# Optimization experiments

Measured on AMD Instinct MI355X. Metric: run time of the kernel, lower is better.

## Reference

```python
import jax, jax.numpy as jnp
import numpy as np

N, C, H, W = 8, 64, 128, 128
KS = 3


def setup_inputs() -> dict:
    key = jax.random.key(0)
    k1, k2, k3, k4 = jax.random.split(key, 4)
    gr = jax.random.normal(k1, (N, C, H, W), dtype=jnp.float32)
    gt = jax.random.normal(k2, (N, C, H, W), dtype=jnp.float32)
    # Conv2d(in_channel, 9*in_channel, 3, stride=1, pad=1): weight [O, I, kh, kw], bias [O]
    fan_in = C * KS * KS
    bound = 1.0 / np.sqrt(fan_in)
    Wc = jax.random.uniform(k3, (KS * KS * C, C, KS, KS), dtype=jnp.float32, minval=-bound, maxval=bound)
    bc = jax.random.uniform(k4, (KS * KS * C,), dtype=jnp.float32, minval=-bound, maxval=bound)
    return {"gr": gr, "gt": gt, "Wc": Wc, "bc": bc}


def reference(gr, gt, Wc, bc):
    # dynamic_filter = Conv2d(C, 9C, 3, 1, 1)(gt)
    filt = jax.lax.conv_general_dilated(
        gt, Wc, window_strides=(1, 1), padding=((1, 1), (1, 1)),
        dimension_numbers=("NCHW", "OIHW", "NCHW"),
    ) + bc[None, :, None, None]  # [N, 9C, H, W]

    n, c, h, w = gr.shape
    pad = (KS - 1) // 2
    # replicate padding (torch F.pad mode='replicate' == jnp 'edge')
    grp = jnp.pad(gr, ((0, 0), (0, 0), (pad, pad), (pad, pad)), mode="edge")
    # 3x3 patches as 9 shifted views: [N, C, 9, H, W], index order (kh, kw)
    patches = jnp.stack(
        [grp[:, :, i:i + h, j:j + w] for i in range(KS) for j in range(KS)], axis=2
    )
    # torch code's conv output channel layout is (c, kh, kw); its double transpose
    # of both patches and kernels cancels, so pairing is kernel[c, kh, kw] * patch[c, kh, kw]
    k = filt.reshape(n, c, KS * KS, h, w)
    return jnp.sum(patches * k, axis=2)  # [N, C, H, W]
```

## Files before the change

### kernel.cpp

```cpp
#include <hip/hip_runtime.h>
#include <stdint.h>


typedef short bf16x8 __attribute__((ext_vector_type(8)));
typedef float f32x4 __attribute__((ext_vector_type(4)));

#define ROWBLK_B 16640
#define BTAP_B   18432
#define ZERO_OFF 663552
#define GTB_OFF  (ZERO_OFF + ROWBLK_B)

__device__ __forceinline__ uint32_t f2bf(float f) {
  uint32_t x = __float_as_uint(f);
  return (x + 0x7FFFu + ((x >> 16) & 1u)) >> 16;
}
__device__ __forceinline__ float bf2f(uint32_t u) { return __uint_as_float(u << 16); }

__device__ __forceinline__ void gload_lds16(const void* g, void* l) {
  __builtin_amdgcn_global_load_lds(
      (const __attribute__((address_space(1))) void*)g,
      (__attribute__((address_space(3))) void*)l, 16, 0, 0);
}

__global__ void prep_wc(const float* __restrict__ Wc, uint8_t* __restrict__ ws) {
  int ch = blockIdx.x * 256 + threadIdx.x;
  int tb = ch / 1152;
  int cw = ch - tb * 1152;
  int tap = tb >> 2, octile = tb & 3;
  int row = cw >> 3, sl = cw & 7;
  int slot = sl ^ (row & 7);
  int ic0 = slot * 8;
  int oc = octile * 144 + row;
  uint32_t p[4];
#pragma unroll
  for (int e = 0; e < 4; ++e) {
    uint32_t lo = f2bf(Wc[(oc * 64 + ic0 + 2 * e) * 9 + tap]);
    uint32_t hi = f2bf(Wc[(oc * 64 + ic0 + 2 * e + 1) * 9 + tap]);
    p[e] = lo | (hi << 16);
  }
  uint4 u; u.x = p[0]; u.y = p[1]; u.z = p[2]; u.w = p[3];
  *(uint4*)(ws + (size_t)tb * BTAP_B + (size_t)cw * 16) = u;
}

__global__ void prep_gt(const float* __restrict__ gt, uint8_t* __restrict__ ws) {
  int b = blockIdx.x;
  if (b == 1024) {
    uint4 z; z.x = z.y = z.z = z.w = 0;
    for (int i = threadIdx.x; i < 1040; i += 256)
      *(uint4*)(ws + ZERO_OFF + (size_t)i * 16) = z;
    return;
  }
  int n = b >> 7, y = b & 127;
  uint8_t* base = ws + GTB_OFF + (size_t)b * ROWBLK_B;
  for (int i = threadIdx.x; i < 1040; i += 256) {
    int r = i >> 3, sl = i & 7;
    int slot = sl ^ (r & 7);
    uint4 u; u.x = u.y = u.z = u.w = 0;
    if (r >= 1 && r <= 128) {
      int w = r - 1, ic0 = slot * 8;
      uint32_t p[4];
#pragma unroll
      for (int e = 0; e < 4; ++e) {
        uint32_t lo = f2bf(gt[((n * 64 + ic0 + 2 * e) * 128 + y) * 128 + w]);
        uint32_t hi = f2bf(gt[((n * 64 + ic0 + 2 * e + 1) * 128 + y) * 128 + w]);
        p[e] = lo | (hi << 16);
      }
      u.x = p[0]; u.y = p[1]; u.z = p[2]; u.w = p[3];
    }
    *(uint4*)(base + (size_t)i * 16) = u;
  }
}

__global__ __launch_bounds__(512, 2) void dfn_mfma(
    const float* __restrict__ gr, const float* __restrict__ bc,
    const uint8_t* __restrict__ ws, float* __restrict__ out) {
  __shared__ uint8_t smem[156928];
  uint8_t* Abuf = smem;
  uint8_t* Bbuf = smem + 83200;
  const int tid = threadIdx.x;
  const int lane = tid & 63;
  const int wv = tid >> 6;
  const int l15 = lane & 15;
  const int l4 = lane >> 4;
  const int bid = blockIdx.x;
  const int octile = (bid >> 3) & 3;
  const int nh = (bid & 7) | ((bid >> 5) << 3);
  const int n = nh >> 5;
  const int h0 = (nh & 31) * 4;

  f32x4 acc[4][9];
#pragma unroll
  for (int nf = 0; nf < 9; ++nf) {
    float bias = bc[octile * 144 + nf * 16 + l15];
#pragma unroll
    for (int mf = 0; mf < 4; ++mf) {
      acc[mf][nf][0] = bias; acc[mf][nf][1] = bias;
      acc[mf][nf][2] = bias; acc[mf][nf][3] = bias;
    }
  }

  int bo[2], aoff[3][2];
#pragma unroll
  for (int kk = 0; kk < 2; ++kk) {
    bo[kk] = l15 * 128 + ((kk * 64 + l4 * 16) ^ ((l15 & 7) << 4));
#pragma unroll
    for (int dwp = 0; dwp < 3; ++dwp) {
      int rl = l15 + dwp;
      aoff[dwp][kk] = rl * 128 + ((kk * 64 + l4 * 16) ^ ((rl & 7) << 4));
    }
  }
  int mrow[4], mcol[4];
#pragma unroll
  for (int mf = 0; mf < 4; ++mf) {
    mrow[mf] = (wv * 4 + mf) >> 3;
    mcol[mf] = ((wv * 4 + mf) & 7) * 2048;
  }

  const uint8_t* gtb = ws + GTB_OFF;
  const uint8_t* zblk = ws + ZERO_OFF;

#define ISSUE_B(T, BUFI) do {                                                 \
    const uint8_t* bsrc_ = ws + (size_t)((T) * 4 + octile) * BTAP_B;          \
    uint8_t* bdst_ = Bbuf + (BUFI) * BTAP_B;                                  \
    _Pragma("unroll")                                                         \
    for (int it = 0; it < 3; ++it) {                                          \
      int idx = it * 512 + tid;                                               \
      if (idx < 1152)                                                         \
        gload_lds16(bsrc_ + (size_t)idx * 16,                                 \
                    bdst_ + (size_t)(it * 512 + (tid & ~63)) * 16);           \
    }                                                                         \
  } while (0)

#define ISSUE_AROW(Y, SLOT) do {                                              \
    int y_ = (Y);                                                             \
    const uint8_t* src_ = (y_ >= 0 && y_ < 128)                               \
        ? (gtb + (size_t)(n * 128 + y_) * ROWBLK_B) : zblk;                   \
    uint8_t* dst_ = Abuf + (SLOT) * ROWBLK_B;                                 \
    _Pragma("unroll")                                                         \
    for (int it = 0; it < 3; ++it) {                                          \
      int idx = it * 512 + tid;                                               \
      if (idx < 1040)                                                         \
        gload_lds16(src_ + (size_t)idx * 16,                                  \
                    dst_ + (size_t)(it * 512 + (tid & ~63)) * 16);            \
    }                                                                         \
  } while (0)

#define TAP(DH, DWP, BUFI) do {                                               \
    const uint8_t* Bcur_ = Bbuf + (BUFI) * BTAP_B;                            \
    _Pragma("unroll")                                                         \
    for (int kk = 0; kk < 2; ++kk) {                                          \
      bf16x8 afr[4];                                                          \
      _Pragma("unroll")                                                       \
      for (int mf = 0; mf < 4; ++mf) {                                        \
        int idx_ = mrow[mf] + ((DH) + 1);                           \
        int slot_ = (idx_ == 5) ? 0 : idx_;     \
        afr[mf] = *(const bf16x8*)(Abuf + slot_ * ROWBLK_B + mcol[mf]         \
                                   + aoff[DWP][kk]);                          \
      }                                                                       \
      const uint8_t* baddr_ = Bcur_ + bo[kk];                                 \
      bf16x8 bq[4];                                                           \
      _Pragma("unroll")                                                       \
      for (int p = 0; p < 4; ++p)                                             \
        bq[p] = *(const bf16x8*)(baddr_ + p * 2048);                          \
      __builtin_amdgcn_s_setprio(1);                                          \
      _Pragma("unroll")                                                       \
      for (int nf = 0; nf < 9; ++nf) {                                        \
        bf16x8 bcur_ = bq[nf & 3];                                            \
        if (nf + 4 < 9)                                                       \
          bq[nf & 3] = *(const bf16x8*)(baddr_ + (nf + 4) * 2048);            \
        _Pragma("unroll")                                                     \
        for (int mf = 0; mf < 4; ++mf)                                        \
          acc[mf][nf] = __builtin_amdgcn_mfma_f32_16x16x32_bf16(              \
              afr[mf], bcur_, acc[mf][nf], 0, 0, 0);                          \
      }                                                                       \
      __builtin_amdgcn_s_setprio(0);                                          \
    }                                                                         \
  } while (0)

#pragma unroll
  for (int row = 0; row < 5; ++row) ISSUE_AROW(h0 - 1 + row, row);
  ISSUE_B(0, 0);
  ISSUE_B(1, 1);
  __syncthreads();

  ISSUE_B(2, 2); ISSUE_B(3, 3);
  TAP(-1, 0, 0); TAP(-1, 1, 1);
  __syncthreads();
  ISSUE_B(4, 0); ISSUE_B(5, 1);
  TAP(-1, 2, 2); TAP(0, 0, 3);
  __syncthreads();
  ISSUE_B(6, 2); ISSUE_B(7, 3);
  ISSUE_AROW(h0 + 4, 0);
  TAP(0, 1, 0); TAP(0, 2, 1);
  __syncthreads();
  ISSUE_B(8, 0);
  TAP(1, 0, 2); TAP(1, 1, 3);
  __syncthreads();
  TAP(1, 2, 0);
  __syncthreads();

  uint8_t* wreg = smem + wv * 8448;
#pragma unroll
  for (int mf = 0; mf < 4; ++mf) {
#pragma unroll
    for (int nf = 0; nf < 9; ++nf) {
      int ocl = nf * 16 + l15;
      int c = (ocl * 7282) >> 16;
      int k = ocl - c * 9;
      uint8_t* wp = wreg + c * 32 + k * 2;
#pragma unroll
      for (int q = 0; q < 4; ++q) {
        int pix = l4 * 4 + q;
        *(uint16_t*)(wp + pix * 528) = (uint16_t)f2bf(acc[mf][nf][q]);
      }
    }
    asm volatile("s_waitcnt lgkmcnt(0)" ::: "memory");
    __builtin_amdgcn_sched_barrier(0);
    int m = (wv * 4 + mf) * 16 + l15;
    int row = m >> 7, w = m & 127;
    int h = h0 + row;
#pragma unroll
    for (int cc = 0; cc < 4; ++cc) {
      int cl = l4 * 4 + cc;
      const uint8_t* rp = wreg + (size_t)l15 * 528 + cl * 32;
      uint4 v0 = *(const uint4*)rp;
      uint32_t v1 = *(const uint32_t*)(rp + 16);
      float fk[9];
      fk[0] = bf2f(v0.x & 0xffff); fk[1] = bf2f(v0.x >> 16);
      fk[2] = bf2f(v0.y & 0xffff); fk[3] = bf2f(v0.y >> 16);
      fk[4] = bf2f(v0.z & 0xffff); fk[5] = bf2f(v0.z >> 16);
      fk[6] = bf2f(v0.w & 0xffff); fk[7] = bf2f(v0.w >> 16);
      fk[8] = bf2f(v1 & 0xffff);
      int cg = octile * 16 + cl;
      const float* grc = gr + (size_t)(n * 64 + cg) * 16384;
      float s = 0.f;
#pragma unroll
      for (int i = 0; i < 3; ++i) {
        int yy = h + i - 1; yy = yy < 0 ? 0 : (yy > 127 ? 127 : yy);
#pragma unroll
        for (int j = 0; j < 3; ++j) {
          int xx = w + j - 1; xx = xx < 0 ? 0 : (xx > 127 ? 127 : xx);
          s = fmaf(fk[i * 3 + j], grc[yy * 128 + xx], s);
        }
      }
      out[(size_t)(n * 64 + cg) * 16384 + h * 128 + w] = s;
    }
    asm volatile("s_waitcnt lgkmcnt(0)" ::: "memory");
    __builtin_amdgcn_sched_barrier(0);
  }
}

extern "C" void kernel_launch(void* const* d_in, const int* in_sizes, int n_in,
                              void* d_out, int out_size, void* d_ws, size_t ws_size,
                              hipStream_t stream) {
  const float* gr = (const float*)d_in[0];
  const float* gt = (const float*)d_in[1];
  const float* Wc = (const float*)d_in[2];
  const float* bc = (const float*)d_in[3];
  uint8_t* ws = (uint8_t*)d_ws;
  float* out = (float*)d_out;

  prep_wc<<<162, 256, 0, stream>>>(Wc, ws);
  prep_gt<<<1025, 256, 0, stream>>>(gt, ws);
  dfn_mfma<<<1024, 512, 0, stream>>>(gr, bc, ws, out);
}
```

Before: 103.6 us.

## Permute filter output channels and swap MFMA operands to skip LDS epilogue transpose

Filter output channels are reordered in the weight prep so each 16-wide N fragment holds one tap across 16 channels. The MFMA operands are swapped so every lane's accumulator directly holds all nine taps for its own pixel and four channels. The epilogue then multiplies against gr straight from registers, with no bf16 round-trip through LDS, no extra barrier and no lgkm waits. This removes the shared-memory transpose and the bf16 rounding of the filter, and it changes the bias load pattern to per-element scalar loads.

```diff
diff --git a/kernel.cpp b/kernel.cpp
--- a/kernel.cpp
+++ b/kernel.cpp
@@ -14,7 +14,6 @@
   uint32_t x = __float_as_uint(f);
   return (x + 0x7FFFu + ((x >> 16) & 1u)) >> 16;
 }
-__device__ __forceinline__ float bf2f(uint32_t u) { return __uint_as_float(u << 16); }
 
 __device__ __forceinline__ void gload_lds16(const void* g, void* l) {
   __builtin_amdgcn_global_load_lds(
@@ -30,7 +29,7 @@
   int row = cw >> 3, sl = cw & 7;
   int slot = sl ^ (row & 7);
   int ic0 = slot * 8;
-  int oc = octile * 144 + row;
+  int oc = octile * 144 + (row & 15) * 9 + (row >> 4);
   uint32_t p[4];
 #pragma unroll
   for (int e = 0; e < 4; ++e) {
@@ -87,17 +86,6 @@
   const int nh = (bid & 7) | ((bid >> 5) << 3);
   const int n = nh >> 5;
   const int h0 = (nh & 31) * 4;
-
-  f32x4 acc[4][9];
-#pragma unroll
-  for (int nf = 0; nf < 9; ++nf) {
-    float bias = bc[octile * 144 + nf * 16 + l15];
-#pragma unroll
-    for (int mf = 0; mf < 4; ++mf) {
-      acc[mf][nf][0] = bias; acc[mf][nf][1] = bias;
-      acc[mf][nf][2] = bias; acc[mf][nf][3] = bias;
-    }
-  }
 
   int bo[2], aoff[3][2];
 #pragma unroll
@@ -171,7 +159,7 @@
         _Pragma("unroll")                                                     \
         for (int mf = 0; mf < 4; ++mf)                                        \
           acc[mf][nf] = __builtin_amdgcn_mfma_f32_16x16x32_bf16(              \
-              afr[mf], bcur_, acc[mf][nf], 0, 0, 0);                          \
+              bcur_, afr[mf], acc[mf][nf], 0, 0, 0);                          \
       }                                                                       \
       __builtin_amdgcn_s_setprio(0);                                          \
     }                                                                         \
@@ -181,6 +169,17 @@
   for (int row = 0; row < 5; ++row) ISSUE_AROW(h0 - 1 + row, row);
   ISSUE_B(0, 0);
   ISSUE_B(1, 1);
+
+  f32x4 acc[4][9];
+#pragma unroll
+  for (int nf = 0; nf < 9; ++nf) {
+#pragma unroll
+    for (int q = 0; q < 4; ++q) {
+      float bias = bc[octile * 144 + (l4 * 4 + q) * 9 + nf];
+      acc[0][nf][q] = bias; acc[1][nf][q] = bias;
+      acc[2][nf][q] = bias; acc[3][nf][q] = bias;
+    }
+  }
   __syncthreads();
 
   ISSUE_B(2, 2); ISSUE_B(3, 3);
@@ -197,56 +196,35 @@
   TAP(1, 0, 2); TAP(1, 1, 3);
   __syncthreads();
   TAP(1, 2, 0);
-  __syncthreads();
-
-  uint8_t* wreg = smem + wv * 8448;
+
+  const float* grb = gr + (size_t)(n * 64 + octile * 16 + l4 * 4) * 16384;
+  float* outb = out + (size_t)(n * 64 + octile * 16 + l4 * 4) * 16384;
 #pragma unroll
   for (int mf = 0; mf < 4; ++mf) {
-#pragma unroll
-    for (int nf = 0; nf < 9; ++nf) {
-      int ocl = nf * 16 + l15;
-      int c = (ocl * 7282) >> 16;
-      int k = ocl - c * 9;
-      uint8_t* wp = wreg + c * 32 + k * 2;
-#pragma unroll
-      for (int q = 0; q < 4; ++q) {
-        int pix = l4 * 4 + q;
-        *(uint16_t*)(wp + pix * 528) = (uint16_t)f2bf(acc[mf][nf][q]);
+    int p = (wv * 4 + mf) * 16 + l15;
+    int hrow = p >> 7, w = p & 127;
+    int h = h0 + hrow;
+    int off[3][3];
+#pragma unroll
+    for (int i = 0; i < 3; ++i) {
+      int yy = h + i - 1; yy = yy < 0 ? 0 : (yy > 127 ? 127 : yy);
+#pragma unroll
+      for (int j = 0; j < 3; ++j) {
+        int xx = w + j - 1; xx = xx < 0 ? 0 : (xx > 127 ? 127 : xx);
+        off[i][j] = yy * 128 + xx;
       }
     }
-    asm volatile("s_waitcnt lgkmcnt(0)" ::: "memory");
-    __builtin_amdgcn_sched_barrier(0);
-    int m = (wv * 4 + mf) * 16 + l15;
-    int row = m >> 7, w = m & 127;
-    int h = h0 + row;
-#pragma unroll
-    for (int cc = 0; cc < 4; ++cc) {
-      int cl = l4 * 4 + cc;
-      const uint8_t* rp = wreg + (size_t)l15 * 528 + cl * 32;
-      uint4 v0 = *(const uint4*)rp;
-      uint32_t v1 = *(const uint32_t*)(rp + 16);
-      float fk[9];
-      fk[0] = bf2f(v0.x & 0xffff); fk[1] = bf2f(v0.x >> 16);
-      fk[2] = bf2f(v0.y & 0xffff); fk[3] = bf2f(v0.y >> 16);
-      fk[4] = bf2f(v0.z & 0xffff); fk[5] = bf2f(v0.z >> 16);
-      fk[6] = bf2f(v0.w & 0xffff); fk[7] = bf2f(v0.w >> 16);
-      fk[8] = bf2f(v1 & 0xffff);
-      int cg = octile * 16 + cl;
-      const float* grc = gr + (size_t)(n * 64 + cg) * 16384;
+#pragma unroll
+    for (int q = 0; q < 4; ++q) {
+      const float* grc = grb + (size_t)q * 16384;
       float s = 0.f;
 #pragma unroll
-      for (int i = 0; i < 3; ++i) {
-        int yy = h + i - 1; yy = yy < 0 ? 0 : (yy > 127 ? 127 : yy);
-#pragma unroll
-        for (int j = 0; j < 3; ++j) {
-          int xx = w + j - 1; xx = xx < 0 ? 0 : (xx > 127 ? 127 : xx);
-          s = fmaf(fk[i * 3 + j], grc[yy * 128 + xx], s);
-        }
-      }
-      out[(size_t)(n * 64 + cg) * 16384 + h * 128 + w] = s;
-    }
-    asm volatile("s_waitcnt lgkmcnt(0)" ::: "memory");
-    __builtin_amdgcn_sched_barrier(0);
+      for (int i = 0; i < 3; ++i)
+#pragma unroll
+        for (int j = 0; j < 3; ++j)
+          s = fmaf(acc[mf][i * 3 + j][q], grc[off[i][j]], s);
+      outb[(size_t)q * 16384 + h * 128 + w] = s;
+    }
   }
 }
 
```

Measured after the change: 96.54 us. -6.8%, faster.
